# Optimization experiments

Measured on AMD Instinct MI355X. Metric: run time of the kernel, lower is better.

The kernel has to match this reference:

```python
import jax, jax.numpy as jnp
import numpy as np

B, T, D_IN = 64, 512, 1024
DENSE = 1024
H = 768
N_INTENTS = 60


def _flip(x, lengths):
    # reverse the first `length` steps of each sequence, keep padding in place
    t = jnp.arange(x.shape[1])[None, :]
    L = lengths[:, None]
    idx = jnp.where(t < L, L - 1 - t, t)  # [B,T]
    return jnp.take_along_axis(x, idx[:, :, None], axis=1)


def _lstm(x, lengths, Wi, Wh, b):
    # x: [B,T,D]; flax OptimizedLSTMCell: gates (i,f,g,o), carry frozen past seq length
    Bb, Tt, _ = x.shape
    Hh = Wh.shape[0]
    xp = jnp.einsum('btd,dk->tbk', x, Wi)  # precompute input proj, time-major [T,B,4H]
    mask = jnp.arange(Tt)[:, None] < lengths[None, :]  # [T,B]

    def step(carry, inp):
        c, h = carry
        xpt, m = inp
        z = xpt + h @ Wh + b
        i, f, g, o = jnp.split(z, 4, axis=-1)
        nc = jax.nn.sigmoid(f) * c + jax.nn.sigmoid(i) * jnp.tanh(g)
        nh = jax.nn.sigmoid(o) * jnp.tanh(nc)
        m1 = m[:, None]
        return (jnp.where(m1, nc, c), jnp.where(m1, nh, h)), nh

    init = (jnp.zeros((Bb, Hh), x.dtype), jnp.zeros((Bb, Hh), x.dtype))
    _, ys = jax.lax.scan(step, init, (xp, mask))
    return ys.transpose(1, 0, 2)  # [B,T,H]


def _bilstm(x, lengths, Wi_f, Wh_f, b_f, Wi_b, Wh_b, b_b):
    yf = _lstm(x, lengths, Wi_f, Wh_f, b_f)
    yb = _flip(_lstm(_flip(x, lengths), lengths, Wi_b, Wh_b, b_b), lengths)
    return jnp.concatenate([yf, yb], axis=-1)


def setup_inputs() -> dict:
    key = jax.random.key(0)
    ks = jax.random.split(key, 24)
    s = 0.02
    p = {}
    p['full_lattice'] = jax.random.normal(ks[0], (B, T, D_IN), jnp.float32)
    p['num_frames'] = jax.random.randint(ks[1], (B,), T // 2, T + 1)
    p['is_test'] = 1
    p['W_reg'] = jax.random.normal(ks[2], (D_IN, DENSE), jnp.float32) * s
    p['b_reg'] = jnp.zeros((DENSE,), jnp.float32)
    d0, d1 = DENSE, 2 * H
    p['Wi0f'] = jax.random.normal(ks[3], (d0, 4 * H)) * s
    p['Wh0f'] = jax.random.normal(ks[4], (H, 4 * H)) * s
    p['b0f'] = jnp.zeros((4 * H,), jnp.float32)
    p['Wi0b'] = jax.random.normal(ks[5], (d0, 4 * H)) * s
    p['Wh0b'] = jax.random.normal(ks[6], (H, 4 * H)) * s
    p['b0b'] = jnp.zeros((4 * H,), jnp.float32)
    p['Wi1f'] = jax.random.normal(ks[7], (d1, 4 * H)) * s
    p['Wh1f'] = jax.random.normal(ks[8], (H, 4 * H)) * s
    p['b1f'] = jnp.zeros((4 * H,), jnp.float32)
    p['Wi1b'] = jax.random.normal(ks[9], (d1, 4 * H)) * s
    p['Wh1b'] = jax.random.normal(ks[10], (H, 4 * H)) * s
    p['b1b'] = jnp.zeros((4 * H,), jnp.float32)
    p['W_keys'] = jax.random.normal(ks[11], (2 * H, 2 * H)) * s
    p['W_energy'] = jax.random.normal(ks[12], (2 * H, 1)) * s
    p['W_post'] = jax.random.normal(ks[13], (2 * H, 2 * H)) * s
    p['b_post'] = jnp.zeros((2 * H,), jnp.float32)
    p['W_int'] = jax.random.normal(ks[14], (2 * H, N_INTENTS)) * s
    p['b_int'] = jnp.zeros((N_INTENTS,), jnp.float32)
    return p


def reference(full_lattice, num_frames, is_test, W_reg, b_reg,
              Wi0f, Wh0f, b0f, Wi0b, Wh0b, b0b,
              Wi1f, Wh1f, b1f, Wi1b, Wh1b, b1b,
              W_keys, W_energy, W_post, b_post, W_int, b_int):
    # regrouping head
    reg = full_lattice @ W_reg + b_reg  # [B,T,DENSE]
    enc = _bilstm(reg, num_frames, Wi0f, Wh0f, b0f, Wi0b, Wh0b, b0b)  # [B,T,2H]
    # dropout deterministic (is_test=True) -> identity
    enc = _bilstm(enc, num_frames, Wi1f, Wh1f, b1f, Wi1b, Wh1b, b1b)  # [B,T,2H]
    mask = jnp.arange(enc.shape[-2])[None, :] < num_frames[:, None]  # [B,T]
    # keys-only MLP (Bahdanau) attention
    energy = jnp.tanh(enc @ W_keys)
    scores = (energy @ W_energy)[..., 0]  # [B,T]
    scores = jnp.where(mask, scores, -jnp.inf)
    attn = jax.nn.softmax(scores, axis=-1)
    context = jnp.einsum('BT,BTH->BH', attn, enc)
    context = context @ W_post + b_post
    intents = context @ W_int + b_int  # [B,N_INTENTS]
    return intents
```

## Files before the change

### kernel.cpp

```cpp
#include <hip/hip_runtime.h>
#include <cstdint>
#include <cstddef>


typedef __attribute__((ext_vector_type(8))) short s8v;
typedef __attribute__((ext_vector_type(4))) short s4v;
typedef __attribute__((ext_vector_type(4))) float f4v;
typedef __attribute__((ext_vector_type(4))) int   v4i;

#define MFMA16(a,b,c) __builtin_amdgcn_mfma_f32_16x16x32_bf16((a),(b),(c),0,0,0)

#define NB   64
#define NT   512
#define MTOT (NB*NT)
#define TC   32

__device__ __forceinline__ ushort f2bf(float x){
  uint32_t u = __float_as_uint(x);
  uint32_t r = (u + 0x7FFFu + ((u >> 16) & 1u)) >> 16;
  return (ushort)r;
}
__device__ __forceinline__ float bf2f(ushort h){
  return __uint_as_float(((uint32_t)h) << 16);
}
__device__ __forceinline__ float fsig(float x){
  x = fminf(30.f, fmaxf(-30.f, x));
  return 1.f / (1.f + __expf(-x));
}
__device__ __forceinline__ float ftanh(float x){
  x = fminf(15.f, fmaxf(-15.f, x));
  float e = __expf(2.f * x);
  return (e - 1.f) / (e + 1.f);
}
__device__ __forceinline__ s8v as8(v4i x){ union{v4i a; s8v b;} u; u.a=x; return u.b; }

__global__ void transpose_split_kernel(const float* __restrict__ B,
                                       ushort* __restrict__ Th,
                                       ushort* __restrict__ Tl,
                                       int K, int N){
  __shared__ float tile[64][65];
  int k0 = blockIdx.x * 64, n0 = blockIdx.y * 64;
  for (int i = threadIdx.x; i < 4096; i += 256){
    int r = i >> 6, c = i & 63;
    tile[r][c] = B[(size_t)(k0 + r) * N + (n0 + c)];
  }
  __syncthreads();
  for (int i = threadIdx.x; i < 4096; i += 256){
    int nr = i >> 6, kc = i & 63;
    float x = tile[kc][nr];
    ushort h = f2bf(x);
    ushort lo = f2bf(x - bf2f(h));
    size_t o = (size_t)(n0 + nr) * K + (k0 + kc);
    Th[o] = h; Tl[o] = lo;
  }
}

__global__ void whpack_kernel(const float* __restrict__ Wh,
                              ushort* __restrict__ Ph, ushort* __restrict__ Pl){
  int idx = blockIdx.x * 256 + threadIdx.x;
  int j    = idx & 7;
  int lane = (idx >> 3) & 63;
  int kt   = (idx >> 9) % 24;
  int rest = idx / (24 * 512);
  int nt   = rest & 1;
  int wgd  = rest >> 1;
  int c    = lane & 15;
  int gate = nt * 2 + (c >> 3);
  int q    = wgd * 8 + (c & 7);
  int k    = kt * 32 + (lane >> 4) * 8 + j;
  float x = Wh[(size_t)k * 3072 + gate * 768 + q];
  ushort h = f2bf(x);
  Ph[idx] = h;
  Pl[idx] = f2bf(x - bf2f(h));
}

__global__ void pack_wi_kernel(const float* __restrict__ W,
                               ushort* __restrict__ dst, int K){
  int total = 96 * 32 * K;
  for (int idx = blockIdx.x * 256 + threadIdx.x; idx < total; idx += gridDim.x * 256){
    int k = idx % K;
    int rest = idx / K;
    int n = rest & 31, wgd = rest >> 5;
    float x = W[(size_t)k * 3072 + (n >> 3) * 768 + wgd * 8 + (n & 7)];
    dst[idx] = f2bf(x);
  }
}

__global__ void bias_comb_kernel(const float* __restrict__ bf, const float* __restrict__ bb,
                                 const float* __restrict__ Wf, const float* __restrict__ Wb,
                                 const float* __restrict__ breg, int Kb,
                                 float* __restrict__ bc){
  int c = blockIdx.x * 256 + threadIdx.x;
  int d = blockIdx.y;
  const float* b = d ? bb : bf;
  const float* W = d ? Wb : Wf;
  float acc = b[c];
  if (W){
    for (int k = 0; k < Kb; k++) acc += breg[k] * W[(size_t)k * 3072 + c];
  }
  bc[d * 3072 + c] = acc;
}

__global__ void zero_kernel(uint32_t* __restrict__ p, int n){
  for (int i = blockIdx.x * 256 + threadIdx.x; i < n; i += gridDim.x * 256)
    p[i] = 0u;
}

template<int MODE, int ABF>
__global__ __launch_bounds__(256, 2) void gemm_kernel(
    const void* __restrict__ Araw, const ushort* __restrict__ Bh,
    const ushort* __restrict__ Bl, const float* __restrict__ bias,
    float* __restrict__ outF,
    const float* __restrict__ We, float* __restrict__ scores,
    int M, int N, int K)
{
  __shared__ short lA_h[128*40], lA_l[128*40], lB_h[128*40], lB_l[128*40];
  int tid = threadIdx.x, l = tid & 63, w = tid >> 6;
  int wr = w >> 1, wc = w & 1;
  int nbM = M >> 7;
  int mblk = blockIdx.x % nbM, nblk = blockIdx.x / nbM;
  f4v acc[4][4];
  for (int i=0;i<4;i++) for (int j=0;j<4;j++) acc[i][j] = (f4v){0.f,0.f,0.f,0.f};
  int nk = K >> 5;
  const ushort* Bhb = Bh + (size_t)nblk*128*K;
  const ushort* Blb = Bl + (size_t)nblk*128*K;
  int mrow = l & 15, koff = (l >> 4) * 8;
  for (int kt = 0; kt < nk; kt++){
    if (ABF == 0){
      const float* Ab = (const float*)Araw + (size_t)mblk*128*K;
      int c4 = (l & 7) * 4;
      #pragma unroll
      for (int i=0;i<4;i++){
        int r = (w*4 + i)*8 + (l >> 3);
        const float* p = Ab + (size_t)r*K + kt*32 + c4;
        float4 v = *(const float4*)p;
        float xs[4] = {v.x, v.y, v.z, v.w};
        s4v hv, lv;
        #pragma unroll
        for (int j=0;j<4;j++){
          ushort hh = f2bf(xs[j]);
          hv[j] = (short)hh;
          lv[j] = (short)f2bf(xs[j] - bf2f(hh));
        }
        *(s4v*)&lA_h[r*40 + c4] = hv;
        *(s4v*)&lA_l[r*40 + c4] = lv;
      }
    } else {
      const ushort* Ab = (const ushort*)Araw + (size_t)mblk*128*K;
      int k8 = (l & 3) * 8;
      #pragma unroll
      for (int i=0;i<2;i++){
        int r = (w*2 + i)*16 + (l >> 2);
        *(s8v*)&lA_h[r*40 + k8] = *(const s8v*)(Ab + (size_t)r*K + kt*32 + k8);
      }
    }
    {
      int k8 = (l & 3) * 8;
      #pragma unroll
      for (int i=0;i<2;i++){
        int r = (w*2 + i)*16 + (l >> 2);
        size_t o = (size_t)r*K + kt*32 + k8;
        *(s8v*)&lB_h[r*40 + k8] = *(const s8v*)(Bhb + o);
        *(s8v*)&lB_l[r*40 + k8] = *(const s8v*)(Blb + o);
      }
    }
    __syncthreads();
    s8v ah[4], al[4], bh[4], bl[4];
    #pragma unroll
    for (int mt=0;mt<4;mt++){
      int base = (wr*64 + mt*16 + mrow)*40 + koff;
      ah[mt] = *(s8v*)&lA_h[base];
      if (ABF == 0) al[mt] = *(s8v*)&lA_l[base];
    }
    #pragma unroll
    for (int nt=0;nt<4;nt++){
      int base = (wc*64 + nt*16 + mrow)*40 + koff;
      bh[nt] = *(s8v*)&lB_h[base];
      bl[nt] = *(s8v*)&lB_l[base];
    }
    #pragma unroll
    for (int mt=0;mt<4;mt++)
      #pragma unroll
      for (int nt=0;nt<4;nt++){
        acc[mt][nt] = MFMA16(ah[mt], bh[nt], acc[mt][nt]);
        acc[mt][nt] = MFMA16(ah[mt], bl[nt], acc[mt][nt]);
        if (ABF == 0) acc[mt][nt] = MFMA16(al[mt], bh[nt], acc[mt][nt]);
      }
    __syncthreads();
  }
  if (MODE == 2){
    float pre[4][4];
    #pragma unroll
    for (int mt=0;mt<4;mt++) for (int r=0;r<4;r++) pre[mt][r] = 0.f;
    #pragma unroll
    for (int nt=0;nt<4;nt++){
      int colg = nblk*128 + wc*64 + nt*16 + (l & 15);
      float we = We[colg];
      #pragma unroll
      for (int mt=0;mt<4;mt++)
        #pragma unroll
        for (int r=0;r<4;r++)
          pre[mt][r] += ftanh(acc[mt][nt][r]) * we;
    }
    #pragma unroll
    for (int mt=0;mt<4;mt++)
      #pragma unroll
      for (int r=0;r<4;r++){
        float v = pre[mt][r];
        v += __shfl_xor(v, 1); v += __shfl_xor(v, 2);
        v += __shfl_xor(v, 4); v += __shfl_xor(v, 8);
        if ((l & 15) == 0){
          int rowg = mblk*128 + wr*64 + mt*16 + (l>>4)*4 + r;
          atomicAdd(scores + rowg, v);
        }
      }
  } else {
    #pragma unroll
    for (int mt=0;mt<4;mt++)
      #pragma unroll
      for (int nt=0;nt<4;nt++){
        int rowg0 = mblk*128 + wr*64 + mt*16 + (l>>4)*4;
        int colg  = nblk*128 + wc*64 + nt*16 + (l & 15);
        float bv = bias ? bias[colg] : 0.f;
        #pragma unroll
        for (int r=0;r<4;r++){
          float v = acc[mt][nt][r] + bv;
          outF[(size_t)(rowg0 + r)*N + colg] = v;
        }
      }
  }
}

template<int ABF>
__global__ __launch_bounds__(256, 2) void xp_gemm(
    const void* __restrict__ Araw, const ushort* __restrict__ Bp,
    const int* __restrict__ nf, int t0,
    ushort* __restrict__ outB, int K)
{
  __shared__ short lA[128*40], lB[128*40];
  __shared__ int srow[128];
  int tid = threadIdx.x, l = tid & 63, w = tid >> 6;
  int wr = w >> 1, wc = w & 1;
  int mblk = blockIdx.x & 15;
  int nblk = blockIdx.x >> 4;
  int dir = (nblk >= 24) ? 1 : 0;
  if (tid < 128){
    int m = mblk*128 + tid;
    int b = m & 63, tc = m >> 6;
    int t = t0 + tc;
    int r = dir ? (nf[b] - 1 - t) : t;
    r = max(0, min(511, r));
    srow[tid] = b*512 + r;
  }
  __syncthreads();
  f4v acc[4][4];
  for (int i=0;i<4;i++) for (int j=0;j<4;j++) acc[i][j] = (f4v){0.f,0.f,0.f,0.f};
  int nk = K >> 5;
  const ushort* Bb = Bp + (size_t)nblk*128*K;
  int mrow = l & 15, koff = (l >> 4) * 8;
  for (int kt = 0; kt < nk; kt++){
    if (ABF == 2){
      const float* Af = (const float*)Araw;
      int c4 = (l & 7) * 4;
      #pragma unroll
      for (int i=0;i<4;i++){
        int r = (w*4 + i)*8 + (l >> 3);
        const float* p = Af + (size_t)srow[r]*K + kt*32 + c4;
        float4 v = *(const float4*)p;
        s4v hv;
        hv[0] = (short)f2bf(v.x); hv[1] = (short)f2bf(v.y);
        hv[2] = (short)f2bf(v.z); hv[3] = (short)f2bf(v.w);
        *(s4v*)&lA[r*40 + c4] = hv;
      }
    } else {
      const ushort* Au = (const ushort*)Araw;
      int k8 = (l & 3) * 8;
      #pragma unroll
      for (int i=0;i<2;i++){
        int r = (w*2 + i)*16 + (l >> 2);
        *(s8v*)&lA[r*40 + k8] = *(const s8v*)(Au + (size_t)srow[r]*K + kt*32 + k8);
      }
    }
    {
      int k8 = (l & 3) * 8;
      #pragma unroll
      for (int i=0;i<2;i++){
        int r = (w*2 + i)*16 + (l >> 2);
        *(s8v*)&lB[r*40 + k8] = *(const s8v*)(Bb + (size_t)r*K + kt*32 + k8);
      }
    }
    __syncthreads();
    s8v ah[4], bh4[4];
    #pragma unroll
    for (int mt=0;mt<4;mt++) ah[mt] = *(s8v*)&lA[(wr*64 + mt*16 + mrow)*40 + koff];
    #pragma unroll
    for (int nt=0;nt<4;nt++) bh4[nt] = *(s8v*)&lB[(wc*64 + nt*16 + mrow)*40 + koff];
    #pragma unroll
    for (int mt=0;mt<4;mt++)
      #pragma unroll
      for (int nt=0;nt<4;nt++)
        acc[mt][nt] = MFMA16(ah[mt], bh4[nt], acc[mt][nt]);
    __syncthreads();
  }
  #pragma unroll
  for (int mt=0;mt<4;mt++)
    #pragma unroll
    for (int nt=0;nt<4;nt++){
      int rowg0 = mblk*128 + wr*64 + mt*16 + (l>>4)*4;
      int colg  = nblk*128 + wc*64 + nt*16 + (l & 15);
      #pragma unroll
      for (int r=0;r<4;r++)
        outB[(size_t)(rowg0 + r)*6144 + colg] = f2bf(acc[mt][nt][r]);
    }
}

__global__ __launch_bounds__(256, 1) void recur_fused(
    const ushort* __restrict__ xp,
    const ushort* __restrict__ whfh, const ushort* __restrict__ whfl,
    const ushort* __restrict__ whbh, const ushort* __restrict__ whbl,
    const float* __restrict__ bias2, ushort* __restrict__ enc,
    const int* __restrict__ nf, ushort* __restrict__ hstate,
    float* __restrict__ cstate, int* __restrict__ barr,
    int t0, int tEnd)
{
  __shared__ float zlds[9216];
  __shared__ float bcs[32];
  __shared__ int nfs[64];
  const int tid = threadIdx.x, l = tid & 63, w = tid >> 6;
  const int dir = blockIdx.x & 1, wgd = blockIdx.x >> 1, wq0 = wgd * 8;

  if (tid < 64) nfs[tid] = nf[tid];
  if (tid < 32) bcs[tid] = bias2[dir*3072 + (tid>>3)*768 + wq0 + (tid&7)];
  __syncthreads();
  const int gb = tid >> 2, qp = tid & 3, q0 = qp*2;
  const int gL = nfs[gb];
  const int ghidx = gb*768 + wq0 + q0;
  float* cst = cstate + dir * 49152;

  const ushort* wph = dir ? whbh : whfh;
  const ushort* wpl = dir ? whbl : whfl;
  s8v whh[2][6], whl[2][6];
  #pragma unroll
  for (int nt=0;nt<2;nt++)
    for (int i=0;i<6;i++){
      size_t o = ((size_t)((wgd*2 + nt)*24 + (w*6 + i)) * 64 + l) * 8;
      whh[nt][i] = *(const s8v*)(wph + o);
      whl[nt][i] = *(const s8v*)(wpl + o);
    }

  uint32_t hoff[4];
  #pragma unroll
  for (int mt=0;mt<4;mt++)
    hoff[mt] = (uint32_t)(((mt*16 + (l & 15))*768 + w*192 + ((l>>4)*8)) * 2);
  uint64_t hb0 = (uint64_t)(uintptr_t)(hstate + (size_t)(dir*2 + 0)*49152);
  uint64_t hb1 = (uint64_t)(uintptr_t)(hstate + (size_t)(dir*2 + 1)*49152);

  const ushort* xcb = xp + (size_t)gb*6144 + (size_t)(dir*3072 + wgd*32);

  const int wgid = blockIdx.x;
  uint32_t lasth = 0;

  for (int t = t0; t < tEnd; t++){
    if (t > 0 && wgid != 0 && tid == 0){
      while (__hip_atomic_load(barr + 256, __ATOMIC_RELAXED, __HIP_MEMORY_SCOPE_AGENT) < t)
        __builtin_amdgcn_s_sleep(2);
    }
    __syncthreads();
    const int p = t & 1;
    const uint64_t rb = p ? hb1 : hb0;
    const uint64_t wb = p ? hb0 : hb1;

    v4i F[4][6];
    #pragma unroll
    for (int mt=0; mt<4; mt++){
      uint64_t amt = rb + hoff[mt];
      asm volatile(
        "global_load_dwordx4 %0, %6, off sc0 sc1\n\t"
        "global_load_dwordx4 %1, %6, off offset:64 sc0 sc1\n\t"
        "global_load_dwordx4 %2, %6, off offset:128 sc0 sc1\n\t"
        "global_load_dwordx4 %3, %6, off offset:192 sc0 sc1\n\t"
        "global_load_dwordx4 %4, %6, off offset:256 sc0 sc1\n\t"
        "global_load_dwordx4 %5, %6, off offset:320 sc0 sc1"
        : "=&v"(F[mt][0]),"=&v"(F[mt][1]),"=&v"(F[mt][2]),
          "=&v"(F[mt][3]),"=&v"(F[mt][4]),"=&v"(F[mt][5])
        : "v"(amt)
        : "memory");
    }
    const ushort* xrow = xcb + (size_t)(t - t0) * (64*6144);
    uint32_t xq[4];
    #pragma unroll
    for (int g=0; g<4; g++) xq[g] = *(const uint32_t*)(xrow + g*8 + q0);

    asm volatile("s_waitcnt vmcnt(0)"
      : "+v"(F[0][0]),"+v"(F[0][1]),"+v"(F[0][2]),"+v"(F[0][3]),"+v"(F[0][4]),"+v"(F[0][5]),
        "+v"(F[1][0]),"+v"(F[1][1]),"+v"(F[1][2]),"+v"(F[1][3]),"+v"(F[1][4]),"+v"(F[1][5]),
        "+v"(F[2][0]),"+v"(F[2][1]),"+v"(F[2][2]),"+v"(F[2][3]),"+v"(F[2][4]),"+v"(F[2][5]),
        "+v"(F[3][0]),"+v"(F[3][1]),"+v"(F[3][2]),"+v"(F[3][3]),"+v"(F[3][4]),"+v"(F[3][5])
      :
      : "memory");

    f4v acc[4][2];
    #pragma unroll
    for (int mt=0;mt<4;mt++){
      acc[mt][0] = (f4v){0.f,0.f,0.f,0.f};
      acc[mt][1] = (f4v){0.f,0.f,0.f,0.f};
    }
    #pragma unroll
    for (int i=0;i<6;i++){
      #pragma unroll
      for (int mt=0;mt<4;mt++){
        s8v ahh = as8(F[mt][i]);
        acc[mt][0] = MFMA16(ahh, whh[0][i], acc[mt][0]);
        acc[mt][0] = MFMA16(ahh, whl[0][i], acc[mt][0]);
        acc[mt][1] = MFMA16(ahh, whh[1][i], acc[mt][1]);
        acc[mt][1] = MFMA16(ahh, whl[1][i], acc[mt][1]);
      }
    }
    #pragma unroll
    for (int mt=0;mt<4;mt++)
      #pragma unroll
      for (int nt=0;nt<2;nt++){
        int base = (((w*4 + mt)*2 + nt)*16 + (l & 15))*18 + (l>>4)*4;
        zlds[base+0] = acc[mt][nt][0];
        zlds[base+1] = acc[mt][nt][1];
        zlds[base+2] = acc[mt][nt][2];
        zlds[base+3] = acc[mt][nt][3];
      }
    __syncthreads();
    {
      if (t < gL){
        int mt = gb >> 4, row = gb & 15;
        float nhv[2];
        #pragma unroll
        for (int e=0;e<2;e++){
          int q = q0 + e;
          float zg4[4];
          #pragma unroll
          for (int g=0; g<4; g++){
            int nt = g >> 1, c = (g & 1)*8 + q;
            int zb = ((mt*2 + nt)*16 + c)*18 + row;
            zg4[g] = zlds[zb] + zlds[zb+2304] + zlds[zb+4608] + zlds[zb+6912]
                   + bcs[g*8 + q] + bf2f((ushort)(xq[g] >> (16*e)));
          }
          float co = cst[ghidx + e];
          float nc = fsig(zg4[1])*co + fsig(zg4[0])*ftanh(zg4[2]);
          float nh = fsig(zg4[3])*ftanh(nc);
          cst[ghidx + e] = nc;
          nhv[e] = nh;
        }
        ushort h0h = f2bf(nhv[0]), h1h = f2bf(nhv[1]);
        uint32_t pk = (uint32_t)h0h | ((uint32_t)h1h << 16);
        lasth = pk;
        uint64_t sa = wb + (uint32_t)(ghidx * 2);
        asm volatile("global_store_dword %0, %1, off sc0 sc1"
                     :: "v"(sa), "v"(pk) : "memory");
        int r = dir ? (gL - 1 - t) : t;
        *(uint32_t*)&enc[((size_t)gb*512 + r)*1536 + dir*768 + wq0 + q0] = pk;
      } else if (t == gL){
        uint64_t sa = wb + (uint32_t)(ghidx * 2);
        asm volatile("global_store_dword %0, %1, off sc0 sc1"
                     :: "v"(sa), "v"(lasth) : "memory");
      }
    }
    asm volatile("s_waitcnt vmcnt(0)" ::: "memory");
    __syncthreads();
    if (t < 511){
      if (tid == 0)
        __hip_atomic_store(barr + wgid, t + 1, __ATOMIC_RELAXED, __HIP_MEMORY_SCOPE_AGENT);
      if (wgid == 0 && w == 0){
        for (;;){
          int v0 = __hip_atomic_load(barr + l,       __ATOMIC_RELAXED, __HIP_MEMORY_SCOPE_AGENT);
          int v1 = __hip_atomic_load(barr + 64 + l,  __ATOMIC_RELAXED, __HIP_MEMORY_SCOPE_AGENT);
          int v2 = __hip_atomic_load(barr + 128 + l, __ATOMIC_RELAXED, __HIP_MEMORY_SCOPE_AGENT);
          int mn = min(v0, min(v1, v2));
          if (__all(mn >= t + 1)) break;
          __builtin_amdgcn_s_sleep(1);
        }
        if (l == 0)
          __hip_atomic_store(barr + 256, t + 1, __ATOMIC_RELAXED, __HIP_MEMORY_SCOPE_AGENT);
      }
    }
  }
}

__global__ void softmax_kernel(const float* __restrict__ scores,
                               const int* __restrict__ nf,
                               float* __restrict__ attn){
  __shared__ float red[4], red2[4];
  int b = blockIdx.x, tid = threadIdx.x;
  int L = nf[b];
  float v0 = (tid       < L) ? scores[b*512 + tid]       : -1e30f;
  float v1 = (tid + 256 < L) ? scores[b*512 + tid + 256] : -1e30f;
  float mx = fmaxf(v0, v1);
  for (int m=1; m<64; m<<=1) mx = fmaxf(mx, __shfl_xor(mx, m));
  if ((tid & 63) == 0) red[tid >> 6] = mx;
  __syncthreads();
  mx = fmaxf(fmaxf(red[0], red[1]), fmaxf(red[2], red[3]));
  float e0 = (tid       < L) ? __expf(v0 - mx) : 0.f;
  float e1 = (tid + 256 < L) ? __expf(v1 - mx) : 0.f;
  float s = e0 + e1;
  for (int m=1; m<64; m<<=1) s += __shfl_xor(s, m);
  if ((tid & 63) == 0) red2[tid >> 6] = s;
  __syncthreads();
  s = red2[0] + red2[1] + red2[2] + red2[3];
  float inv = 1.f / s;
  attn[b*512 + tid]       = e0 * inv;
  attn[b*512 + tid + 256] = e1 * inv;
}

__global__ void context_kernel(const ushort* __restrict__ enc,
                               const float* __restrict__ attn,
                               float* __restrict__ ctx){
  int b = blockIdx.x, tid = threadIdx.x;
  float a6[6] = {0.f,0.f,0.f,0.f,0.f,0.f};
  for (int t=0; t<512; t++){
    float a = attn[b*512 + t];
    if (a != 0.f){
      const ushort* e = enc + ((size_t)b*512 + t)*1536;
      #pragma unroll
      for (int i=0;i<6;i++) a6[i] += a * bf2f(e[tid + i*256]);
    }
  }
  #pragma unroll
  for (int i=0;i<6;i++) ctx[b*1536 + tid + i*256] = a6[i];
}

__global__ void post_kernel(const float* __restrict__ ctx,
                            const float* __restrict__ Wp,
                            const float* __restrict__ bp,
                            float* __restrict__ post){
  int b = blockIdx.x;
  int j = blockIdx.y*256 + threadIdx.x;
  float acc = bp[j];
  const float* c = ctx + b*1536;
  for (int k=0;k<1536;k++) acc += c[k] * Wp[(size_t)k*1536 + j];
  post[b*1536 + j] = acc;
}

__global__ void intents_kernel(const float* __restrict__ post,
                               const float* __restrict__ Wi,
                               const float* __restrict__ bi,
                               float* __restrict__ out){
  int b = blockIdx.x, j = threadIdx.x;
  if (j < 60){
    float acc = bi[j];
    const float* p = post + b*1536;
    for (int k=0;k<1536;k++) acc += p[k] * Wi[k*60 + j];
    out[b*60 + j] = acc;
  }
}

extern "C" void kernel_launch(void* const* d_in, const int* in_sizes, int n_in,
                              void* d_out, int out_size, void* d_ws, size_t ws_size,
                              hipStream_t stream) {
  const float* lat    = (const float*)d_in[0];
  const int*   nf     = (const int*)  d_in[1];
  const float* W_reg  = (const float*)d_in[3];
  const float* b_reg  = (const float*)d_in[4];
  const float* Wi0f   = (const float*)d_in[5];
  const float* Wh0f   = (const float*)d_in[6];
  const float* b0f    = (const float*)d_in[7];
  const float* Wi0b   = (const float*)d_in[8];
  const float* Wh0b   = (const float*)d_in[9];
  const float* b0b    = (const float*)d_in[10];
  const float* Wi1f   = (const float*)d_in[11];
  const float* Wh1f   = (const float*)d_in[12];
  const float* b1f    = (const float*)d_in[13];
  const float* Wi1b   = (const float*)d_in[14];
  const float* Wh1b   = (const float*)d_in[15];
  const float* b1b    = (const float*)d_in[16];
  const float* W_keys = (const float*)d_in[17];
  const float* W_en   = (const float*)d_in[18];
  const float* W_post = (const float*)d_in[19];
  const float* b_post = (const float*)d_in[20];
  const float* W_int  = (const float*)d_in[21];
  const float* b_int  = (const float*)d_in[22];
  float* out = (float*)d_out;

  char* wsp = (char*)d_ws;
  auto alloc = [&](size_t n) -> char* {
    char* p = wsp; wsp += (n + 255) & ~(size_t)255; return p;
  };
  ushort* enc1 = (ushort*)alloc((size_t)MTOT*1536*2);
  ushort* enc2 = (ushort*)alloc((size_t)MTOT*1536*2);
  ushort* wip  = (ushort*)alloc((size_t)2*96*32*1536*2);
  ushort* wh_fh = (ushort*)alloc((size_t)2359296*2);
  ushort* wh_fl = (ushort*)alloc((size_t)2359296*2);
  ushort* wh_bh = (ushort*)alloc((size_t)2359296*2);
  ushort* wh_bl = (ushort*)alloc((size_t)2359296*2);
  float*  bc   = (float*) alloc((size_t)2*3072*4);
  char* state0 = wsp;
  ushort* hstate = (ushort*)alloc((size_t)4*49152*2);
  float*  cstate = (float*) alloc((size_t)2*49152*4);
  int*    barr   = (int*)   alloc(4096);
  size_t state_bytes = (size_t)((char*)wsp - state0);
  char* U = alloc((size_t)25165824);
  ushort* sTh  = (ushort*)(U);
  ushort* sTl  = (ushort*)(U + 6291456);
  float*  sWc  = (float*) (U + 12582912);
  ushort* xpc  = (ushort*)(U);
  float* scores = (float*)(U + 12582912);
  float* attn   = (float*)(U + 12582912 + 131072);
  float* ctx    = (float*)(U + 12582912 + 262144);
  float* postb  = (float*)(U + 12582912 + 262144 + 393216);
  (void)in_sizes; (void)n_in; (void)out_size; (void)ws_size;

  int state_words = (int)(state_bytes / 4);

  hipLaunchKernelGGL(zero_kernel, dim3(512), dim3(256), 0, stream, (uint32_t*)state0, state_words);
  hipLaunchKernelGGL(transpose_split_kernel, dim3(16,48), dim3(256), 0, stream, Wi0f, sTh, sTl, 1024, 3072);
  hipLaunchKernelGGL((gemm_kernel<0,0>), dim3(8*24), dim3(256), 0, stream,
                     (const void*)W_reg, sTh, sTl, (const float*)nullptr, sWc,
                     (const float*)nullptr, (float*)nullptr, 1024, 3072, 1024);
  hipLaunchKernelGGL(pack_wi_kernel, dim3(4608), dim3(256), 0, stream, sWc, wip, 1024);
  hipLaunchKernelGGL(transpose_split_kernel, dim3(16,48), dim3(256), 0, stream, Wi0b, sTh, sTl, 1024, 3072);
  hipLaunchKernelGGL((gemm_kernel<0,0>), dim3(8*24), dim3(256), 0, stream,
                     (const void*)W_reg, sTh, sTl, (const float*)nullptr, sWc,
                     (const float*)nullptr, (float*)nullptr, 1024, 3072, 1024);
  hipLaunchKernelGGL(pack_wi_kernel, dim3(4608), dim3(256), 0, stream, sWc, wip + (size_t)96*32*1024, 1024);
  hipLaunchKernelGGL(whpack_kernel, dim3(9216), dim3(256), 0, stream, Wh0f, wh_fh, wh_fl);
  hipLaunchKernelGGL(whpack_kernel, dim3(9216), dim3(256), 0, stream, Wh0b, wh_bh, wh_bl);
  hipLaunchKernelGGL(bias_comb_kernel, dim3(12,2), dim3(256), 0, stream, b0f, b0b, Wi0f, Wi0b, b_reg, 1024, bc);
  for (int c = 0; c < 512/TC; c++){
    int t0 = c*TC;
    hipLaunchKernelGGL((xp_gemm<2>), dim3(16*48), dim3(256), 0, stream,
                       (const void*)lat, wip, nf, t0, xpc, 1024);
    hipLaunchKernelGGL(recur_fused, dim3(192), dim3(256), 0, stream,
                       xpc, wh_fh, wh_fl, wh_bh, wh_bl, bc,
                       enc1, nf, hstate, cstate, barr, t0, t0 + TC);
  }
  hipLaunchKernelGGL(zero_kernel, dim3(512), dim3(256), 0, stream, (uint32_t*)state0, state_words);
  hipLaunchKernelGGL(pack_wi_kernel, dim3(4608), dim3(256), 0, stream, Wi1f, wip, 1536);
  hipLaunchKernelGGL(pack_wi_kernel, dim3(4608), dim3(256), 0, stream, Wi1b, wip + (size_t)96*32*1536, 1536);
  hipLaunchKernelGGL(whpack_kernel, dim3(9216), dim3(256), 0, stream, Wh1f, wh_fh, wh_fl);
  hipLaunchKernelGGL(whpack_kernel, dim3(9216), dim3(256), 0, stream, Wh1b, wh_bh, wh_bl);
  hipLaunchKernelGGL(bias_comb_kernel, dim3(12,2), dim3(256), 0, stream, b1f, b1b,
                     (const float*)nullptr, (const float*)nullptr, b_reg, 0, bc);
  for (int c = 0; c < 512/TC; c++){
    int t0 = c*TC;
    hipLaunchKernelGGL((xp_gemm<1>), dim3(16*48), dim3(256), 0, stream,
                       (const void*)enc1, wip, nf, t0, xpc, 1536);
    hipLaunchKernelGGL(recur_fused, dim3(192), dim3(256), 0, stream,
                       xpc, wh_fh, wh_fl, wh_bh, wh_bl, bc,
                       enc2, nf, hstate, cstate, barr, t0, t0 + TC);
  }
  hipLaunchKernelGGL(zero_kernel, dim3(128), dim3(256), 0, stream, (uint32_t*)scores, MTOT);
  hipLaunchKernelGGL(transpose_split_kernel, dim3(24,24), dim3(256), 0, stream, W_keys, sTh, sTl, 1536, 1536);
  hipLaunchKernelGGL((gemm_kernel<2,1>), dim3(256*12), dim3(256), 0, stream,
                     (const void*)enc2, sTh, sTl, (const float*)nullptr, (float*)nullptr,
                     W_en, scores, MTOT, 1536, 1536);
  hipLaunchKernelGGL(softmax_kernel, dim3(64), dim3(256), 0, stream, scores, nf, attn);
  hipLaunchKernelGGL(context_kernel, dim3(64), dim3(256), 0, stream, enc2, attn, ctx);
  hipLaunchKernelGGL(post_kernel, dim3(64,6), dim3(256), 0, stream, ctx, W_post, b_post, postb);
  hipLaunchKernelGGL(intents_kernel, dim3(64), dim3(64), 0, stream, postb, W_int, b_int, out);
}
```

Before: 10.03 ms.

## Use per-direction decentralized barrier, register cell state, skip padded score tiles

Replaces the centralized two-hop grid barrier (every workgroup signals, workgroup 0 aggregates and broadcasts) with a decentralized scheme. Each workgroup's wave 0 polls the 96 flags of its own direction, so forward and backward directions no longer synchronize with each other. The LSTM cell state is kept in registers across the time chunk instead of being read and written in global memory each step. The attention-score GEMM also exits early for 128-row tiles that lie entirely past a sequence's length. Removing the past-length h-state rewrite relies on the freeze semantics still holding through the double-buffered h state, which is a correctness risk. Every workgroup now polling adds memory traffic on the flag lines.

```diff
diff --git a/kernel.cpp b/kernel.cpp
--- a/kernel.cpp
+++ b/kernel.cpp
@@ -112,6 +112,7 @@
     const ushort* __restrict__ Bl, const float* __restrict__ bias,
     float* __restrict__ outF,
     const float* __restrict__ We, float* __restrict__ scores,
+    const int* __restrict__ nf,
     int M, int N, int K)
 {
   __shared__ short lA_h[128*40], lA_l[128*40], lB_h[128*40], lB_l[128*40];
@@ -119,6 +120,10 @@
   int wr = w >> 1, wc = w & 1;
   int nbM = M >> 7;
   int mblk = blockIdx.x % nbM, nblk = blockIdx.x / nbM;
+  if (MODE == 2){
+    int b = mblk >> 2, t0 = (mblk & 3) * 128;
+    if (nf[b] <= t0) return;
+  }
   f4v acc[4][4];
   for (int i=0;i<4;i++) for (int j=0;j<4;j++) acc[i][j] = (f4v){0.f,0.f,0.f,0.f};
   int nk = K >> 5;
@@ -336,6 +341,9 @@
   const int gL = nfs[gb];
   const int ghidx = gb*768 + wq0 + q0;
   float* cst = cstate + dir * 49152;
+  float creg[2];
+  creg[0] = cst[ghidx];
+  creg[1] = cst[ghidx + 1];
 
   const ushort* wph = dir ? whbh : whfh;
   const ushort* wpl = dir ? whbl : whfl;
@@ -357,13 +365,19 @@
 
   const ushort* xcb = xp + (size_t)gb*6144 + (size_t)(dir*3072 + wgd*32);
 
-  const int wgid = blockIdx.x;
-  uint32_t lasth = 0;
+  const int slot = dir*96 + wgd;
+  const int sb   = dir*96;
 
   for (int t = t0; t < tEnd; t++){
-    if (t > 0 && wgid != 0 && tid == 0){
-      while (__hip_atomic_load(barr + 256, __ATOMIC_RELAXED, __HIP_MEMORY_SCOPE_AGENT) < t)
-        __builtin_amdgcn_s_sleep(2);
+    if (t > 0 && w == 0){
+      for (;;){
+        int v0 = __hip_atomic_load(barr + sb + l, __ATOMIC_RELAXED, __HIP_MEMORY_SCOPE_AGENT);
+        int v1 = (l < 32)
+          ? __hip_atomic_load(barr + sb + 64 + l, __ATOMIC_RELAXED, __HIP_MEMORY_SCOPE_AGENT)
+          : 0x7fffffff;
+        if (__all(min(v0, v1) >= t)) break;
+        __builtin_amdgcn_s_sleep(1);
+      }
     }
     __syncthreads();
     const int p = t & 1;
@@ -442,45 +456,27 @@
             zg4[g] = zlds[zb] + zlds[zb+2304] + zlds[zb+4608] + zlds[zb+6912]
                    + bcs[g*8 + q] + bf2f((ushort)(xq[g] >> (16*e)));
           }
-          float co = cst[ghidx + e];
-          float nc = fsig(zg4[1])*co + fsig(zg4[0])*ftanh(zg4[2]);
+          float nc = fsig(zg4[1])*creg[e] + fsig(zg4[0])*ftanh(zg4[2]);
           float nh = fsig(zg4[3])*ftanh(nc);
-          cst[ghidx + e] = nc;
+          creg[e] = nc;
           nhv[e] = nh;
         }
         ushort h0h = f2bf(nhv[0]), h1h = f2bf(nhv[1]);
         uint32_t pk = (uint32_t)h0h | ((uint32_t)h1h << 16);
-        lasth = pk;
         uint64_t sa = wb + (uint32_t)(ghidx * 2);
         asm volatile("global_store_dword %0, %1, off sc0 sc1"
                      :: "v"(sa), "v"(pk) : "memory");
         int r = dir ? (gL - 1 - t) : t;
         *(uint32_t*)&enc[((size_t)gb*512 + r)*1536 + dir*768 + wq0 + q0] = pk;
-      } else if (t == gL){
-        uint64_t sa = wb + (uint32_t)(ghidx * 2);
-        asm volatile("global_store_dword %0, %1, off sc0 sc1"
-                     :: "v"(sa), "v"(lasth) : "memory");
       }
     }
     asm volatile("s_waitcnt vmcnt(0)" ::: "memory");
     __syncthreads();
-    if (t < 511){
-      if (tid == 0)
-        __hip_atomic_store(barr + wgid, t + 1, __ATOMIC_RELAXED, __HIP_MEMORY_SCOPE_AGENT);
-      if (wgid == 0 && w == 0){
-        for (;;){
-          int v0 = __hip_atomic_load(barr + l,       __ATOMIC_RELAXED, __HIP_MEMORY_SCOPE_AGENT);
-          int v1 = __hip_atomic_load(barr + 64 + l,  __ATOMIC_RELAXED, __HIP_MEMORY_SCOPE_AGENT);
-          int v2 = __hip_atomic_load(barr + 128 + l, __ATOMIC_RELAXED, __HIP_MEMORY_SCOPE_AGENT);
-          int mn = min(v0, min(v1, v2));
-          if (__all(mn >= t + 1)) break;
-          __builtin_amdgcn_s_sleep(1);
-        }
-        if (l == 0)
-          __hip_atomic_store(barr + 256, t + 1, __ATOMIC_RELAXED, __HIP_MEMORY_SCOPE_AGENT);
-      }
-    }
-  }
+    if (t < 511 && tid == 0)
+      __hip_atomic_store(barr + slot, t + 1, __ATOMIC_RELAXED, __HIP_MEMORY_SCOPE_AGENT);
+  }
+  cst[ghidx]     = creg[0];
+  cst[ghidx + 1] = creg[1];
 }
 
 __global__ void softmax_kernel(const float* __restrict__ scores,
@@ -611,12 +607,12 @@
   hipLaunchKernelGGL(transpose_split_kernel, dim3(16,48), dim3(256), 0, stream, Wi0f, sTh, sTl, 1024, 3072);
   hipLaunchKernelGGL((gemm_kernel<0,0>), dim3(8*24), dim3(256), 0, stream,
                      (const void*)W_reg, sTh, sTl, (const float*)nullptr, sWc,
-                     (const float*)nullptr, (float*)nullptr, 1024, 3072, 1024);
+                     (const float*)nullptr, (float*)nullptr, (const int*)nullptr, 1024, 3072, 1024);
   hipLaunchKernelGGL(pack_wi_kernel, dim3(4608), dim3(256), 0, stream, sWc, wip, 1024);
   hipLaunchKernelGGL(transpose_split_kernel, dim3(16,48), dim3(256), 0, stream, Wi0b, sTh, sTl, 1024, 3072);
   hipLaunchKernelGGL((gemm_kernel<0,0>), dim3(8*24), dim3(256), 0, stream,
                      (const void*)W_reg, sTh, sTl, (const float*)nullptr, sWc,
-                     (const float*)nullptr, (float*)nullptr, 1024, 3072, 1024);
+                     (const float*)nullptr, (float*)nullptr, (const int*)nullptr, 1024, 3072, 1024);
   hipLaunchKernelGGL(pack_wi_kernel, dim3(4608), dim3(256), 0, stream, sWc, wip + (size_t)96*32*1024, 1024);
   hipLaunchKernelGGL(whpack_kernel, dim3(9216), dim3(256), 0, stream, Wh0f, wh_fh, wh_fl);
   hipLaunchKernelGGL(whpack_kernel, dim3(9216), dim3(256), 0, stream, Wh0b, wh_bh, wh_bl);
@@ -648,7 +644,7 @@
   hipLaunchKernelGGL(transpose_split_kernel, dim3(24,24), dim3(256), 0, stream, W_keys, sTh, sTl, 1536, 1536);
   hipLaunchKernelGGL((gemm_kernel<2,1>), dim3(256*12), dim3(256), 0, stream,
                      (const void*)enc2, sTh, sTl, (const float*)nullptr, (float*)nullptr,
-                     W_en, scores, MTOT, 1536, 1536);
+                     W_en, scores, nf, MTOT, 1536, 1536);
   hipLaunchKernelGGL(softmax_kernel, dim3(64), dim3(256), 0, stream, scores, nf, attn);
   hipLaunchKernelGGL(context_kernel, dim3(64), dim3(256), 0, stream, enc2, attn, ctx);
   hipLaunchKernelGGL(post_kernel, dim3(64,6), dim3(256), 0, stream, ctx, W_post, b_post, postb);
```

Result: slower. 10.82 ms (+7.9%).
